# Kernel tuning notes

Measured on AMD Instinct MI355X. Metric: run time of the kernel, lower is better.

## Reference

```python
import jax, jax.numpy as jnp
import numpy as np

HIDDEN = 512

def setup_inputs() -> dict:
    key = jax.random.key(0)
    ks = jax.random.split(key, 8)
    B, T, H = 64, 2048, HIDDEN
    s_ih = 1.0 / np.sqrt(H)
    inp = {
        'x': jax.random.normal(ks[0], (B, T, 1), dtype=jnp.float32),
        # PyTorch LSTM params, gate order (i, f, g, o)
        'W_ih': jax.random.uniform(ks[1], (4 * H, 1), jnp.float32, -s_ih, s_ih),
        'W_hh': jax.random.uniform(ks[2], (4 * H, H), jnp.float32, -s_ih, s_ih),
        'b_ih': jax.random.uniform(ks[3], (4 * H,), jnp.float32, -s_ih, s_ih),
        'b_hh': jax.random.uniform(ks[4], (4 * H,), jnp.float32, -s_ih, s_ih),
        'W_fc': jax.random.uniform(ks[5], (1, H), jnp.float32, -s_ih, s_ih),
        'b_fc': jax.random.uniform(ks[6], (1,), jnp.float32, -s_ih, s_ih),
    }
    return inp


def _lstm(x, W_ih, W_hh, b_ih, b_hh):
    # x: [B, T, 1] -> scan over time
    B, T, _ = x.shape
    H = W_hh.shape[1]
    # precompute input projection for all timesteps: [T, B, 4H]
    x_proj = jnp.einsum('bti,gi->tbg', x, W_ih) + (b_ih + b_hh)

    def step(carry, xp_t):
        h, c = carry
        gates = xp_t + h @ W_hh.T  # [B, 4H]
        i, f, g, o = jnp.split(gates, 4, axis=-1)
        i = jax.nn.sigmoid(i)
        f = jax.nn.sigmoid(f)
        g = jnp.tanh(g)
        o = jax.nn.sigmoid(o)
        c = f * c + i * g
        h = o * jnp.tanh(c)
        return (h, c), h

    h0 = jnp.zeros((B, H), x.dtype)
    c0 = jnp.zeros((B, H), x.dtype)
    (h_n, c_n), hs = jax.lax.scan(step, (h0, c0), x_proj)
    out = jnp.transpose(hs, (1, 0, 2))  # [B, T, H]
    return out, h_n, c_n


def reference(x, W_ih, W_hh, b_ih, b_hh, W_fc, b_fc):
    out, h_n, c_n = _lstm(x, W_ih, W_hh, b_ih, b_hh)
    y = out @ W_fc.T + b_fc  # [B, T, 1]
    # h_n/c_n shaped [num_layers, B, H] like torch
    return y, h_n[None], c_n[None]
```

## Files before the change

### kernel.cpp

```cpp
#include <hip/hip_runtime.h>


#define TT 2048
#define BB 64
#define HH 512
#define GB 8
#define NBLK 32
#define DEPTH 4
#define PLANE (GB * HH)
#define Y_OFF 0
#define HN_OFF (BB * TT)
#define CN_OFF (BB * TT + BB * HH)

typedef short short8 __attribute__((ext_vector_type(8)));
typedef float f32x4  __attribute__((ext_vector_type(4)));

__device__ __forceinline__ unsigned f2bf(float f) {
    unsigned u = __float_as_uint(f);
    return (u + 0x7fffu + ((u >> 16) & 1u)) >> 16;
}
__device__ __forceinline__ float bf2f(unsigned h) { return __uint_as_float(h << 16); }

__device__ __forceinline__ unsigned ld_agent(const unsigned* p) {
    return __hip_atomic_load(p, __ATOMIC_RELAXED, __HIP_MEMORY_SCOPE_AGENT);
}
__device__ __forceinline__ void st_agent(unsigned* p, unsigned v) {
    __hip_atomic_store(p, v, __ATOMIC_RELAXED, __HIP_MEMORY_SCOPE_AGENT);
}
__device__ __forceinline__ unsigned add_agent(unsigned* p, unsigned v) {
    return __hip_atomic_fetch_add(p, v, __ATOMIC_RELAXED, __HIP_MEMORY_SCOPE_AGENT);
}
__device__ __forceinline__ short8 ld_sc1_b128(const unsigned short* p) {
    unsigned long long q0 = __hip_atomic_load((const unsigned long long*)p,
                                              __ATOMIC_RELAXED, __HIP_MEMORY_SCOPE_AGENT);
    unsigned long long q1 = __hip_atomic_load((const unsigned long long*)(p + 4),
                                              __ATOMIC_RELAXED, __HIP_MEMORY_SCOPE_AGENT);
    union { unsigned long long q[2]; short8 s; } u;
    u.q[0] = q0; u.q[1] = q1;
    return u.s;
}

__device__ __forceinline__ void ld_sc0_8x128(const void* pa, const void* pb,
                                             short8* A, short8* B) {
    asm volatile(
        "global_load_dwordx4 %0, %[pa], off sc0\n\t"
        "global_load_dwordx4 %1, %[pa], off offset:64 sc0\n\t"
        "global_load_dwordx4 %2, %[pa], off offset:128 sc0\n\t"
        "global_load_dwordx4 %3, %[pa], off offset:192 sc0\n\t"
        "global_load_dwordx4 %4, %[pb], off sc0\n\t"
        "global_load_dwordx4 %5, %[pb], off offset:64 sc0\n\t"
        "global_load_dwordx4 %6, %[pb], off offset:128 sc0\n\t"
        "global_load_dwordx4 %7, %[pb], off offset:192 sc0\n\t"
        "s_waitcnt vmcnt(0)"
        : "=&v"(A[0]), "=&v"(A[1]), "=&v"(A[2]), "=&v"(A[3]),
          "=&v"(B[0]), "=&v"(B[1]), "=&v"(B[2]), "=&v"(B[3])
        : [pa] "v"(pa), [pb] "v"(pb)
        : "memory");
}
__device__ __forceinline__ uint4 ld_sc0_probe(const void* p) {
    uint4 d;
    asm volatile("global_load_dwordx4 %0, %1, off sc0\n\ts_waitcnt vmcnt(0)"
                 : "=&v"(d) : "v"(p) : "memory");
    return d;
}

#define GSP(w, tl, r, c) gsp[((((w) * 4 + (tl)) * 16 + (r)) * 20) + (c)]

template <bool FAST>
__device__ __noinline__ void run_loop(
    const float* __restrict__ x, const float* __restrict__ Whh,
    const float* __restrict__ Wih, const float* __restrict__ bih,
    const float* __restrict__ bhh, const float* __restrict__ Wfc,
    const float* __restrict__ bfc, float* __restrict__ out,
    unsigned short* __restrict__ hb, unsigned* __restrict__ stepc,
    const int grp, const int ut, float* gsp)
{
    const int tid  = threadIdx.x;
    const int wid  = tid >> 6;
    const int lane = tid & 63;
    const int quad = lane >> 4;
    const int l16  = lane & 15;

    short8 whi[4][4], wlo[4][4];
#pragma unroll
    for (int tl = 0; tl < 4; ++tl) {
        const int grow  = tl * HH + ut * 16 + l16;
        const float* wr = Whh + grow * HH + wid * 128 + quad * 8;
#pragma unroll
        for (int ki = 0; ki < 4; ++ki) {
            const float* wp = wr + ki * 32;
            short8 h8, l8;
#pragma unroll
            for (int j = 0; j < 8; ++j) {
                const float f = wp[j];
                const unsigned hi = f2bf(f);
                h8[j] = (short)hi;
                l8[j] = (short)f2bf(f - bf2f(hi));
            }
            whi[tl][ki] = h8;
            wlo[tl][ki] = l8;
        }
    }

    const int b2    = (tid >> 4) & 7;
    const int u     = tid & 15;
    const int bglob = grp * GB + b2;
    const int ug    = ut * 16 + u;
    float wih4[4], bia4[4];
#pragma unroll
    for (int gi = 0; gi < 4; ++gi) {
        const int grow = gi * HH + ug;
        wih4[gi] = Wih[grow];
        bia4[gi] = bih[grow] + bhh[grow];
    }
    const float wfc  = Wfc[ug];
    const float bfcv = bfc[0];
    float c = 0.0f;

    const int base_hi = grp * 2 * DEPTH;
    const int base_lo = base_hi + DEPTH;
    unsigned* hb32 = (unsigned*)hb;
    const unsigned* pollp = stepc + (tid & 31);

    for (int t = 0; t < TT; ++t) {
        if (tid < 64) {
            const unsigned tgt = (unsigned)t;
            for (;;) {
                const unsigned v = ld_agent(pollp);
                if (__all((int)(v >= tgt))) break;
            }
        }
        __syncthreads();

        const float xv = x[bglob * TT + t];

        const unsigned short* Ah =
            hb + (base_hi + (t & 3)) * PLANE + (l16 & 7) * HH + wid * 128 + quad * 8;
        const unsigned short* Al =
            hb + (base_lo + (t & 3)) * PLANE + (l16 & 7) * HH + wid * 128 + quad * 8;
        short8 ah[4], al[4];
        if constexpr (FAST) {
            ld_sc0_8x128(Ah, Al, ah, al);
        } else {
#pragma unroll
            for (int ki = 0; ki < 4; ++ki) {
                ah[ki] = ld_sc1_b128(Ah + ki * 32);
                al[ki] = ld_sc1_b128(Al + ki * 32);
            }
        }

        f32x4 acc[4] = {{0.f,0.f,0.f,0.f},{0.f,0.f,0.f,0.f},
                        {0.f,0.f,0.f,0.f},{0.f,0.f,0.f,0.f}};
#pragma unroll
        for (int ki = 0; ki < 4; ++ki) {
#pragma unroll
            for (int tl = 0; tl < 4; ++tl)
                acc[tl] = __builtin_amdgcn_mfma_f32_16x16x32_bf16(ah[ki], whi[tl][ki], acc[tl], 0, 0, 0);
#pragma unroll
            for (int tl = 0; tl < 4; ++tl)
                acc[tl] = __builtin_amdgcn_mfma_f32_16x16x32_bf16(al[ki], whi[tl][ki], acc[tl], 0, 0, 0);
#pragma unroll
            for (int tl = 0; tl < 4; ++tl)
                acc[tl] = __builtin_amdgcn_mfma_f32_16x16x32_bf16(ah[ki], wlo[tl][ki], acc[tl], 0, 0, 0);
        }
#pragma unroll
        for (int tl = 0; tl < 4; ++tl)
#pragma unroll
            for (int r = 0; r < 4; ++r)
                GSP(wid, tl, quad * 4 + r, l16) = acc[tl][r];
        __syncthreads();

        if (tid < 128) {
            float pre[4];
#pragma unroll
            for (int gi = 0; gi < 4; ++gi) {
                float s = 0.f;
#pragma unroll
                for (int w = 0; w < 4; ++w) s += GSP(w, gi, b2, u);
                pre[gi] = fmaf(xv, wih4[gi], bia4[gi]) + s;
            }
            const float ig = 1.f / (1.f + __expf(-pre[0]));
            const float fg = 1.f / (1.f + __expf(-pre[1]));
            const float gg = 2.f / (1.f + __expf(-2.f * pre[2])) - 1.f;
            const float og = 1.f / (1.f + __expf(-pre[3]));
            c = fmaf(fg, c, ig * gg);
            const float tc = 2.f / (1.f + __expf(-2.f * c)) - 1.f;
            const float h  = og * tc;

            const unsigned hh = f2bf(h);
            const unsigned hl = f2bf(h - bf2f(hh));
            const unsigned packed = hh | (hl << 16);
            const unsigned part = (unsigned)__shfl_xor((int)packed, 1, 64);
            if ((u & 1) == 0) {
                const unsigned sH = __builtin_amdgcn_perm(part, packed, 0x05040100u);
                const unsigned sL = __builtin_amdgcn_perm(part, packed, 0x07060302u);
                const int slot    = (t + 1) & 3;
                const int pairidx = (b2 * HH + ug) >> 1;
                if constexpr (FAST) {
                    __hip_atomic_store(hb32 + (base_hi + slot) * (PLANE / 2) + pairidx, sH,
                                       __ATOMIC_RELAXED, __HIP_MEMORY_SCOPE_WORKGROUP);
                    __hip_atomic_store(hb32 + (base_lo + slot) * (PLANE / 2) + pairidx, sL,
                                       __ATOMIC_RELAXED, __HIP_MEMORY_SCOPE_WORKGROUP);
                } else {
                    __hip_atomic_store(hb32 + (base_hi + slot) * (PLANE / 2) + pairidx, sH,
                                       __ATOMIC_RELAXED, __HIP_MEMORY_SCOPE_AGENT);
                    __hip_atomic_store(hb32 + (base_lo + slot) * (PLANE / 2) + pairidx, sL,
                                       __ATOMIC_RELAXED, __HIP_MEMORY_SCOPE_AGENT);
                }
            }

            float yp = h * wfc;
            yp += __shfl_down(yp, 8, 16);
            yp += __shfl_down(yp, 4, 16);
            yp += __shfl_down(yp, 2, 16);
            yp += __shfl_down(yp, 1, 16);
            if (u == 0) {
                if (ut == 0) yp += bfcv;
                if constexpr (FAST)
                    __hip_atomic_fetch_add(out + Y_OFF + bglob * TT + t, yp,
                                           __ATOMIC_RELAXED, __HIP_MEMORY_SCOPE_WORKGROUP);
                else
                    atomicAdd(out + Y_OFF + bglob * TT + t, yp);
            }
            if (t == TT - 1) {
                out[HN_OFF + bglob * HH + ug] = h;
                out[CN_OFF + bglob * HH + ug] = c;
            }
        }
        __syncthreads();
        if (tid == 0) st_agent(stepc + ut, (unsigned)(t + 1));
    }
}

__global__ __launch_bounds__(256, 1)
void lstm_xcd(const float* __restrict__ x, const float* __restrict__ Wih,
              const float* __restrict__ Whh, const float* __restrict__ bih,
              const float* __restrict__ bhh, const float* __restrict__ Wfc,
              const float* __restrict__ bfc, float* __restrict__ out,
              unsigned short* __restrict__ hb, unsigned* __restrict__ cnt)
{
    __shared__ int s_grp, s_ut, s_fast;
    __shared__ float gsp[4 * 4 * 16 * 20];

    const int tid = threadIdx.x;
    unsigned* claim = cnt + 512;
    unsigned* bar1  = cnt + 544;

    if (tid == 0) {
        unsigned xcc;
        asm volatile("s_getreg_b32 %0, hwreg(HW_REG_XCC_ID)" : "=s"(xcc));
        xcc &= 7u;
        const unsigned slot = add_agent(claim + xcc, 1u);
        asm volatile("s_waitcnt vmcnt(0)" ::: "memory");
        add_agent(bar1, 1u);
        while (ld_agent(bar1) < 256u) __builtin_amdgcn_s_sleep(1);
        bool pure = true;
        for (int g2 = 0; g2 < 8; ++g2) pure &= (ld_agent(claim + g2) == (unsigned)NBLK);

        int fast = 0, grp, ut;
        if (pure) {
            grp = (int)xcc; ut = (int)slot;
            unsigned* probe = cnt + 1024 + grp * 32;
            unsigned* pflag = cnt + 1280 + grp * 32;
            unsigned* v_ok  = cnt + 1536 + grp * 32;
            unsigned* v_tot = cnt + 1792 + grp * 32;
            if (ut == 0) {
                uint4 m = make_uint4(0xC0FFEE42u, 0x5EED5EEDu, 0xA110C8EDu, 0xB16B00B5u);
                *(uint4*)probe = m;
                asm volatile("s_waitcnt vmcnt(0)" ::: "memory");
                st_agent(pflag, 1u);
            }
            while (ld_agent(pflag) == 0u) __builtin_amdgcn_s_sleep(1);
            const uint4 d = ld_sc0_probe(probe);
            const unsigned ok = (d.x == 0xC0FFEE42u && d.y == 0x5EED5EEDu &&
                                 d.z == 0xA110C8EDu && d.w == 0xB16B00B5u) ? 1u : 0u;
            add_agent(v_ok, ok);
            asm volatile("s_waitcnt vmcnt(0)" ::: "memory");
            add_agent(v_tot, 1u);
            while (ld_agent(v_tot) < (unsigned)NBLK) __builtin_amdgcn_s_sleep(1);
            fast = (ld_agent(v_ok) == (unsigned)NBLK) ? 1 : 0;
        } else {
            grp = (int)(blockIdx.x >> 5); ut = (int)(blockIdx.x & 31);
        }
        s_grp = grp; s_ut = ut; s_fast = fast;
    }
    __syncthreads();
    const int grp = s_grp, ut = s_ut;
    unsigned* stepc = cnt + grp * 32;

    if (s_fast) run_loop<true >(x, Whh, Wih, bih, bhh, Wfc, bfc, out, hb, stepc, grp, ut, gsp);
    else        run_loop<false>(x, Whh, Wih, bih, bhh, Wfc, bfc, out, hb, stepc, grp, ut, gsp);
}

extern "C" void kernel_launch(void* const* d_in, const int* in_sizes, int n_in,
                              void* d_out, int out_size, void* d_ws, size_t ws_size,
                              hipStream_t stream) {
    const float* x   = (const float*)d_in[0];
    const float* Wih = (const float*)d_in[1];
    const float* Whh = (const float*)d_in[2];
    const float* bih = (const float*)d_in[3];
    const float* bhh = (const float*)d_in[4];
    const float* Wfc = (const float*)d_in[5];
    const float* bfc = (const float*)d_in[6];
    float* out = (float*)d_out;

    unsigned*       cnt = (unsigned*)d_ws;
    unsigned short* hb  = (unsigned short*)((char*)d_ws + 16384);

    hipMemsetAsync(d_ws, 0, 16384 + 8 * 2 * DEPTH * PLANE * sizeof(unsigned short), stream);
    hipMemsetAsync(d_out, 0, BB * TT * sizeof(float), stream);

    lstm_xcd<<<dim3(256), dim3(256), 0, stream>>>(
        x, Wih, Whh, bih, bhh, Wfc, bfc, out, hb, cnt);
}
```

Baseline: 5.914 ms.

## Use single L2 atomic counter barrier and defer FC output reduction to separate kernel

```diff
diff --git a/kernel.cpp b/kernel.cpp
--- a/kernel.cpp
+++ b/kernel.cpp
@@ -11,6 +11,9 @@
 #define Y_OFF 0
 #define HN_OFF (BB * TT)
 #define CN_OFF (BB * TT + BB * HH)
+#define RING_OFF 16384
+#define PART_OFF (16384 + 524288)
+#define PART_BYTES (8 * NBLK * GB * TT * 4)
 
 typedef short short8 __attribute__((ext_vector_type(8)));
 typedef float f32x4  __attribute__((ext_vector_type(4)));
@@ -38,6 +41,17 @@
     union { unsigned long long q[2]; short8 s; } u;
     u.q[0] = q0; u.q[1] = q1;
     return u.s;
+}
+
+__device__ __forceinline__ unsigned l2_poll_rmw(unsigned* p) {
+    unsigned ret;
+    asm volatile("global_atomic_add %0, %1, %2, off sc0\n\t"
+                 "s_waitcnt vmcnt(0)"
+                 : "=&v"(ret) : "v"(p), "v"(0u) : "memory");
+    return ret;
+}
+__device__ __forceinline__ void l2_signal_add(unsigned* p, unsigned v) {
+    asm volatile("global_atomic_add %0, %1, off" :: "v"(p), "v"(v) : "memory");
 }
 
 __device__ __forceinline__ void ld_sc0_8x128(const void* pa, const void* pb,
@@ -72,7 +86,8 @@
     const float* __restrict__ Wih, const float* __restrict__ bih,
     const float* __restrict__ bhh, const float* __restrict__ Wfc,
     const float* __restrict__ bfc, float* __restrict__ out,
-    unsigned short* __restrict__ hb, unsigned* __restrict__ stepc,
+    unsigned short* __restrict__ hb, unsigned* __restrict__ done,
+    float* __restrict__ party,
     const int grp, const int ut, float* gsp)
 {
     const int tid  = threadIdx.x;
@@ -120,14 +135,14 @@
     const int base_hi = grp * 2 * DEPTH;
     const int base_lo = base_hi + DEPTH;
     unsigned* hb32 = (unsigned*)hb;
-    const unsigned* pollp = stepc + (tid & 31);
 
     for (int t = 0; t < TT; ++t) {
-        if (tid < 64) {
-            const unsigned tgt = (unsigned)t;
-            for (;;) {
-                const unsigned v = ld_agent(pollp);
-                if (__all((int)(v >= tgt))) break;
+        if (tid == 0) {
+            const unsigned tgt = (unsigned)t * 32u;
+            if constexpr (FAST) {
+                while (l2_poll_rmw(done) < tgt) {}
+            } else {
+                while (ld_agent(done) < tgt) __builtin_amdgcn_s_sleep(1);
             }
         }
         __syncthreads();
@@ -196,17 +211,12 @@
                 const unsigned sL = __builtin_amdgcn_perm(part, packed, 0x07060302u);
                 const int slot    = (t + 1) & 3;
                 const int pairidx = (b2 * HH + ug) >> 1;
-                if constexpr (FAST) {
-                    __hip_atomic_store(hb32 + (base_hi + slot) * (PLANE / 2) + pairidx, sH,
-                                       __ATOMIC_RELAXED, __HIP_MEMORY_SCOPE_WORKGROUP);
-                    __hip_atomic_store(hb32 + (base_lo + slot) * (PLANE / 2) + pairidx, sL,
-                                       __ATOMIC_RELAXED, __HIP_MEMORY_SCOPE_WORKGROUP);
-                } else {
-                    __hip_atomic_store(hb32 + (base_hi + slot) * (PLANE / 2) + pairidx, sH,
-                                       __ATOMIC_RELAXED, __HIP_MEMORY_SCOPE_AGENT);
-                    __hip_atomic_store(hb32 + (base_lo + slot) * (PLANE / 2) + pairidx, sL,
-                                       __ATOMIC_RELAXED, __HIP_MEMORY_SCOPE_AGENT);
-                }
+                const int scope   = FAST ? __HIP_MEMORY_SCOPE_WORKGROUP
+                                         : __HIP_MEMORY_SCOPE_AGENT;
+                __hip_atomic_store(hb32 + (base_hi + slot) * (PLANE / 2) + pairidx, sH,
+                                   __ATOMIC_RELAXED, scope);
+                __hip_atomic_store(hb32 + (base_lo + slot) * (PLANE / 2) + pairidx, sL,
+                                   __ATOMIC_RELAXED, scope);
             }
 
             float yp = h * wfc;
@@ -215,12 +225,12 @@
             yp += __shfl_down(yp, 2, 16);
             yp += __shfl_down(yp, 1, 16);
             if (u == 0) {
-                if (ut == 0) yp += bfcv;
-                if constexpr (FAST)
-                    __hip_atomic_fetch_add(out + Y_OFF + bglob * TT + t, yp,
-                                           __ATOMIC_RELAXED, __HIP_MEMORY_SCOPE_WORKGROUP);
-                else
+                if (party) {
+                    party[((grp * NBLK + ut) * GB + b2) * TT + t] = yp;
+                } else {
+                    if (ut == 0) yp += bfcv;
                     atomicAdd(out + Y_OFF + bglob * TT + t, yp);
+                }
             }
             if (t == TT - 1) {
                 out[HN_OFF + bglob * HH + ug] = h;
@@ -228,7 +238,10 @@
             }
         }
         __syncthreads();
-        if (tid == 0) st_agent(stepc + ut, (unsigned)(t + 1));
+        if (tid == 0) {
+            if constexpr (FAST) l2_signal_add(done, 1u);
+            else                add_agent(done, 1u);
+        }
     }
 }
 
@@ -237,7 +250,8 @@
               const float* __restrict__ Whh, const float* __restrict__ bih,
               const float* __restrict__ bhh, const float* __restrict__ Wfc,
               const float* __restrict__ bfc, float* __restrict__ out,
-              unsigned short* __restrict__ hb, unsigned* __restrict__ cnt)
+              unsigned short* __restrict__ hb, unsigned* __restrict__ cnt,
+              float* __restrict__ party)
 {
     __shared__ int s_grp, s_ut, s_fast;
     __shared__ float gsp[4 * 4 * 16 * 20];
@@ -260,20 +274,24 @@
         int fast = 0, grp, ut;
         if (pure) {
             grp = (int)xcc; ut = (int)slot;
-            unsigned* probe = cnt + 1024 + grp * 32;
-            unsigned* pflag = cnt + 1280 + grp * 32;
-            unsigned* v_ok  = cnt + 1536 + grp * 32;
-            unsigned* v_tot = cnt + 1792 + grp * 32;
+            unsigned* pat   = cnt + 1024 + grp * 64;
+            unsigned* pdone = cnt + 1536 + grp * 64;
+            unsigned* pflag = cnt + 2048 + grp * 32;
+            unsigned* v_ok  = cnt + 2304 + grp * 32;
+            unsigned* v_tot = cnt + 2560 + grp * 32;
             if (ut == 0) {
                 uint4 m = make_uint4(0xC0FFEE42u, 0x5EED5EEDu, 0xA110C8EDu, 0xB16B00B5u);
-                *(uint4*)probe = m;
+                *(uint4*)pat = m;
+                l2_signal_add(pdone, 5u);
                 asm volatile("s_waitcnt vmcnt(0)" ::: "memory");
                 st_agent(pflag, 1u);
             }
             while (ld_agent(pflag) == 0u) __builtin_amdgcn_s_sleep(1);
-            const uint4 d = ld_sc0_probe(probe);
+            const uint4 d     = ld_sc0_probe(pat);
+            const unsigned dv = l2_poll_rmw(pdone);
             const unsigned ok = (d.x == 0xC0FFEE42u && d.y == 0x5EED5EEDu &&
-                                 d.z == 0xA110C8EDu && d.w == 0xB16B00B5u) ? 1u : 0u;
+                                 d.z == 0xA110C8EDu && d.w == 0xB16B00B5u &&
+                                 dv == 5u) ? 1u : 0u;
             add_agent(v_ok, ok);
             asm volatile("s_waitcnt vmcnt(0)" ::: "memory");
             add_agent(v_tot, 1u);
@@ -286,10 +304,24 @@
     }
     __syncthreads();
     const int grp = s_grp, ut = s_ut;
-    unsigned* stepc = cnt + grp * 32;
-
-    if (s_fast) run_loop<true >(x, Whh, Wih, bih, bhh, Wfc, bfc, out, hb, stepc, grp, ut, gsp);
-    else        run_loop<false>(x, Whh, Wih, bih, bhh, Wfc, bfc, out, hb, stepc, grp, ut, gsp);
+    unsigned* done = cnt + grp * 64;
+
+    if (s_fast) run_loop<true >(x, Whh, Wih, bih, bhh, Wfc, bfc, out, hb, done, party, grp, ut, gsp);
+    else        run_loop<false>(x, Whh, Wih, bih, bhh, Wfc, bfc, out, hb, done, party, grp, ut, gsp);
+}
+
+__global__ __launch_bounds__(256)
+void yred(const float* __restrict__ party, const float* __restrict__ bfc,
+          float* __restrict__ out)
+{
+    const int i = blockIdx.x * 256 + threadIdx.x;
+    const int b = i >> 11, t = i & 2047;
+    const int g = b >> 3, lb = b & 7;
+    const float* p = party + ((g * NBLK) * GB + lb) * TT + t;
+    float s = bfc[0];
+#pragma unroll 8
+    for (int ut = 0; ut < NBLK; ++ut) s += p[ut * GB * TT];
+    out[Y_OFF + b * TT + t] = s;
 }
 
 extern "C" void kernel_launch(void* const* d_in, const int* in_sizes, int n_in,
@@ -305,11 +337,15 @@
     float* out = (float*)d_out;
 
     unsigned*       cnt = (unsigned*)d_ws;
-    unsigned short* hb  = (unsigned short*)((char*)d_ws + 16384);
-
-    hipMemsetAsync(d_ws, 0, 16384 + 8 * 2 * DEPTH * PLANE * sizeof(unsigned short), stream);
+    unsigned short* hb  = (unsigned short*)((char*)d_ws + RING_OFF);
+    const bool use_part = ws_size >= (size_t)PART_OFF + PART_BYTES;
+    float* party = use_part ? (float*)((char*)d_ws + PART_OFF) : nullptr;
+
+    hipMemsetAsync(d_ws, 0, RING_OFF + 8 * 2 * DEPTH * PLANE * sizeof(unsigned short), stream);
     hipMemsetAsync(d_out, 0, BB * TT * sizeof(float), stream);
 
     lstm_xcd<<<dim3(256), dim3(256), 0, stream>>>(
-        x, Wih, Whh, bih, bhh, Wfc, bfc, out, hb, cnt);
-}
+        x, Wih, Whh, bih, bhh, Wfc, bfc, out, hb, cnt, party);
+    if (use_part)
+        yred<<<dim3(BB * TT / 256), dim3(256), 0, stream>>>(party, bfc, out);
+}
```

Result: slower. 6.445 ms (+9.0%).
